# Optimization experiments

Hardware: AMD Instinct MI355X
Metric: run time of the kernel (lower is better)

## Reference

```python
import jax, jax.numpy as jnp
import numpy as np

B, T, D, H = 2, 2048, 1024, 16
HD = D // H
DFF = 4 * D
EPS = 1e-5


def gelu_tanh(x):
    c = jnp.sqrt(2.0 / jnp.pi).astype(x.dtype)
    return 0.5 * x * (1.0 + jnp.tanh(c * (x + 0.044715 * x ** 3)))


def layernorm(x, scale, shift):
    mean = jnp.mean(x, axis=-1, keepdims=True)
    var = jnp.var(x, axis=-1, keepdims=True)  # unbiased=False
    return (x - mean) / jnp.sqrt(var + EPS) * scale + shift


def setup_inputs() -> dict:
    key = jax.random.key(0)
    ks = jax.random.split(key, 12)
    s = lambda fan_in: 1.0 / np.sqrt(fan_in)
    return {
        "x": jax.random.normal(ks[0], (B, T, D), jnp.float32),
        "wq": jax.random.normal(ks[1], (D, D), jnp.float32) * s(D),
        "wk": jax.random.normal(ks[2], (D, D), jnp.float32) * s(D),
        "wv": jax.random.normal(ks[3], (D, D), jnp.float32) * s(D),
        "wo": jax.random.normal(ks[4], (D, D), jnp.float32) * s(D),
        "bo": jnp.zeros((D,), jnp.float32),
        "ln1_scale": jnp.ones((D,), jnp.float32),
        "ln1_shift": jnp.zeros((D,), jnp.float32),
        "ln2_scale": jnp.ones((D,), jnp.float32),
        "ln2_shift": jnp.zeros((D,), jnp.float32),
        "w1": jax.random.normal(ks[5], (D, DFF), jnp.float32) * s(D),
        "b1": jnp.zeros((DFF,), jnp.float32),
        "w2": jax.random.normal(ks[6], (DFF, D), jnp.float32) * s(DFF),
        "b2": jnp.zeros((D,), jnp.float32),
    }


def reference(x, wq, wk, wv, wo, bo, ln1_scale, ln1_shift, ln2_scale, ln2_shift, w1, b1, w2, b2):
    # pre-LN attention
    h = layernorm(x, ln1_scale, ln1_shift)
    q = (h @ wq).reshape(B, T, H, HD).transpose(0, 2, 1, 3)  # [B,H,T,hd]
    k = (h @ wk).reshape(B, T, H, HD).transpose(0, 2, 1, 3)
    v = (h @ wv).reshape(B, T, H, HD).transpose(0, 2, 1, 3)
    scores = jnp.einsum('bhqd,bhkd->bhqk', q, k) / jnp.sqrt(jnp.float32(HD))
    causal = jnp.tril(jnp.ones((T, T), bool))
    scores = jnp.where(causal, scores, -jnp.inf)
    attn = jax.nn.softmax(scores, axis=-1)
    ctx = jnp.einsum('bhqk,bhkd->bhqd', attn, v)
    ctx = ctx.transpose(0, 2, 1, 3).reshape(B, T, D)
    attn_out = ctx @ wo + bo
    x = x + attn_out  # dropout p=0
    # pre-LN FFN
    h2 = layernorm(x, ln2_scale, ln2_shift)
    ff = gelu_tanh(h2 @ w1 + b1) @ w2 + b2
    return x + ff
```

## Files before the change

### kernel.cpp

```cpp
#include <hip/hip_runtime.h>
#include <hip/hip_bf16.h>
#include <stdint.h>

typedef unsigned short u16;
typedef __attribute__((ext_vector_type(8))) short s16x8;
typedef __attribute__((ext_vector_type(4))) float f32x4;

#define B_   2
#define T_   2048
#define D_   1024
#define H_   16
#define HD_  64
#define DFF_ 4096
#define M_   (B_*T_)

#define SC2F 0.18033688f

__device__ __forceinline__ u16 f2b(float f){
  uint32_t u = __float_as_uint(f);
  u += 0x7FFFu + ((u >> 16) & 1u);
  return (u16)(u >> 16);
}
__device__ __forceinline__ float b2f(u16 u){ return __uint_as_float(((uint32_t)u) << 16); }
__device__ __forceinline__ uint32_t pk2(float lo, float hi){
  uint32_t r;
  asm volatile("v_cvt_pk_bf16_f32 %0, %1, %2" : "=v"(r) : "v"(lo), "v"(hi));
  return r;
}

__device__ __forceinline__ void gl_lds16(const void* g, void* l){
  __builtin_amdgcn_global_load_lds((const __attribute__((address_space(1))) void*)g,
                                   (__attribute__((address_space(3))) void*)l, 16, 0, 0);
}

template<int N> __device__ __forceinline__ void waitvm(){
  if constexpr (N == 0)      asm volatile("s_waitcnt vmcnt(0)" ::: "memory");
  else if constexpr (N == 2) asm volatile("s_waitcnt vmcnt(2)" ::: "memory");
  else if constexpr (N == 4) asm volatile("s_waitcnt vmcnt(4)" ::: "memory");
  else                       asm volatile("s_waitcnt vmcnt(8)" ::: "memory");
}

__device__ __forceinline__ void wconv_tile(const float* __restrict__ W, u16* __restrict__ Wt,
                                           int K, int N, int tk, int tn, int tid,
                                           u16* __restrict__ tile ){
  const int k0 = tk << 6, n0 = tn << 6;
  const int rr = tid >> 4, c4 = (tid & 15) << 2;
  #pragma unroll
  for (int rep = 0; rep < 4; rep++){
    int r = rr + (rep << 4);
    float4 v = *reinterpret_cast<const float4*>(W + (size_t)(k0 + r)*N + n0 + c4);
    tile[r*68 + c4+0] = f2b(v.x); tile[r*68 + c4+1] = f2b(v.y);
    tile[r*68 + c4+2] = f2b(v.z); tile[r*68 + c4+3] = f2b(v.w);
  }
  __syncthreads();
  const int rn = tid >> 2, kb = (tid & 3) << 4;
  u16 tmp[16];
  #pragma unroll
  for (int j = 0; j < 16; j++) tmp[j] = tile[(kb + j)*68 + rn];
  ushort4* dst = reinterpret_cast<ushort4*>(Wt + (size_t)(n0 + rn)*K + k0 + kb);
  dst[0] = make_ushort4(tmp[0], tmp[1], tmp[2], tmp[3]);
  dst[1] = make_ushort4(tmp[4], tmp[5], tmp[6], tmp[7]);
  dst[2] = make_ushort4(tmp[8], tmp[9], tmp[10], tmp[11]);
  dst[3] = make_ushort4(tmp[12], tmp[13], tmp[14], tmp[15]);
}

__global__ __launch_bounds__(256) void wconv_all(const float* __restrict__ wq,
                                                 const float* __restrict__ wk,
                                                 const float* __restrict__ wv,
                                                 const float* __restrict__ wo,
                                                 u16* __restrict__ wqkvT, u16* __restrict__ woT,
                                                 const float* __restrict__ x,
                                                 const float* __restrict__ ln1s,
                                                 const float* __restrict__ ln1b,
                                                 u16* __restrict__ hout){
  const int bid = blockIdx.x;
  const int tid = threadIdx.x;
  if (bid >= 1024){
    const int row = bid - 1024;
    float4 a = reinterpret_cast<const float4*>(x + ((size_t)row << 10))[tid];
    float s = a.x + a.y + a.z + a.w;
    float q = a.x*a.x + a.y*a.y + a.z*a.z + a.w*a.w;
    #pragma unroll
    for (int o = 32; o > 0; o >>= 1){ s += __shfl_xor(s, o); q += __shfl_xor(q, o); }
    __shared__ float red[8];
    const int w = tid >> 6;
    if ((tid & 63) == 0){ red[w] = s; red[4 + w] = q; }
    __syncthreads();
    float S = red[0] + red[1] + red[2] + red[3];
    float Q = red[4] + red[5] + red[6] + red[7];
    float mean = S * (1.0f/1024.0f);
    float var  = Q * (1.0f/1024.0f) - mean*mean;
    float inv = rsqrtf(var + 1e-5f);
    float4 gsc = reinterpret_cast<const float4*>(ln1s)[tid];
    float4 gsh = reinterpret_cast<const float4*>(ln1b)[tid];
    ushort4 o4;
    o4.x = f2b((a.x - mean)*inv*gsc.x + gsh.x);
    o4.y = f2b((a.y - mean)*inv*gsc.y + gsh.y);
    o4.z = f2b((a.z - mean)*inv*gsc.z + gsh.z);
    o4.w = f2b((a.w - mean)*inv*gsc.w + gsh.w);
    reinterpret_cast<ushort4*>(hout + ((size_t)row << 10))[tid] = o4;
    return;
  }
  __shared__ u16 tile[64*68];
  const int which = bid >> 8, t = bid & 255;
  const float* W = (which == 0) ? wq : (which == 1) ? wk : (which == 2) ? wv : wo;
  u16* Wt = (which == 3) ? woT : wqkvT + (size_t)which * D_ * D_;
  wconv_tile(W, Wt, 1024, 1024, t >> 4, t & 15, tid, tile);
}

__global__ __launch_bounds__(256) void reduce2(const u16* __restrict__ p,
                                               const float* __restrict__ bias,
                                               const u16* __restrict__ resid,
                                               float* __restrict__ out){
  const size_t idx = ((size_t)blockIdx.x << 8) + threadIdx.x;
  ushort4 a4 = reinterpret_cast<const ushort4*>(p)[idx];
  ushort4 b4 = reinterpret_cast<const ushort4*>(p)[idx + (((size_t)M_*D_) >> 2)];
  ushort4 r4 = reinterpret_cast<const ushort4*>(resid)[idx];
  float4 bb = reinterpret_cast<const float4*>(bias)[threadIdx.x];
  float4 o;
  o.x = b2f(a4.x) + b2f(b4.x) + b2f(r4.x) + bb.x;
  o.y = b2f(a4.y) + b2f(b4.y) + b2f(r4.y) + bb.y;
  o.z = b2f(a4.z) + b2f(b4.z) + b2f(r4.z) + bb.z;
  o.w = b2f(a4.w) + b2f(b4.w) + b2f(r4.w) + bb.w;
  reinterpret_cast<float4*>(out)[idx] = o;
}

__global__ __launch_bounds__(256) void reduce_ln(const u16* __restrict__ p,
                                                 const float* __restrict__ bias,
                                                 const float* __restrict__ resid,
                                                 const float* __restrict__ sc,
                                                 const float* __restrict__ sh,
                                                 u16* __restrict__ x1,
                                                 u16* __restrict__ h2){
  const int row = blockIdx.x;
  const int tid = threadIdx.x;
  const size_t idx = ((size_t)row << 8) + tid;
  ushort4 a4 = reinterpret_cast<const ushort4*>(p)[idx];
  ushort4 b4 = reinterpret_cast<const ushort4*>(p)[idx + (((size_t)M_*D_) >> 2)];
  float4 r  = reinterpret_cast<const float4*>(resid)[idx];
  float4 bb = reinterpret_cast<const float4*>(bias)[tid];
  float4 v;
  v.x = b2f(a4.x) + b2f(b4.x) + r.x + bb.x;
  v.y = b2f(a4.y) + b2f(b4.y) + r.y + bb.y;
  v.z = b2f(a4.z) + b2f(b4.z) + r.z + bb.z;
  v.w = b2f(a4.w) + b2f(b4.w) + r.w + bb.w;
  ushort4 xo;
  xo.x = f2b(v.x); xo.y = f2b(v.y); xo.z = f2b(v.z); xo.w = f2b(v.w);
  reinterpret_cast<ushort4*>(x1)[idx] = xo;
  float s = v.x + v.y + v.z + v.w;
  float q = v.x*v.x + v.y*v.y + v.z*v.z + v.w*v.w;
  #pragma unroll
  for (int o = 32; o > 0; o >>= 1){ s += __shfl_xor(s, o); q += __shfl_xor(q, o); }
  __shared__ float red[8];
  const int w = tid >> 6;
  if ((tid & 63) == 0){ red[w] = s; red[4 + w] = q; }
  __syncthreads();
  float S = red[0] + red[1] + red[2] + red[3];
  float Q = red[4] + red[5] + red[6] + red[7];
  float mean = S * (1.0f/1024.0f);
  float var  = Q * (1.0f/1024.0f) - mean*mean;
  float inv = rsqrtf(var + 1e-5f);
  float4 gsc = reinterpret_cast<const float4*>(sc)[tid];
  float4 gsh = reinterpret_cast<const float4*>(sh)[tid];
  ushort4 o4;
  o4.x = f2b((v.x - mean)*inv*gsc.x + gsh.x);
  o4.y = f2b((v.y - mean)*inv*gsc.y + gsh.y);
  o4.z = f2b((v.z - mean)*inv*gsc.z + gsh.z);
  o4.w = f2b((v.w - mean)*inv*gsc.w + gsh.w);
  reinterpret_cast<ushort4*>(h2 + ((size_t)row << 10))[tid] = o4;
}

template<int EPI, int NF>
__global__ __launch_bounds__(512, 2) void gemm8(const u16* __restrict__ A, const u16* __restrict__ Bt,
                                                const float* __restrict__ bias,
                                                void* __restrict__ Cv, void* __restrict__ Cv2,
                                                const float* __restrict__ cw1,
                                                const float* __restrict__ cw2,
                                                u16* __restrict__ w1T, u16* __restrict__ w2T,
                                                int M, int N, int K, int lda){
  constexpr int BROWS = NF * 32;
  __shared__ __align__(16) u16 LA[2][2][128*64];
  __shared__ __align__(16) u16 LB[2][2][BROWS*64];
  const int tid = threadIdx.x;

  if constexpr (EPI == 1){
    if (blockIdx.x >= 192){
      const int tid256 = tid & 255, sel2 = tid >> 8;
      u16* tile = &LA[0][0][0] + sel2 * (64*68);
      const int t = ((int)blockIdx.x - 192)*2 + sel2;
      if (t < 1024) wconv_tile(cw1, w1T, 1024, 4096, t >> 6, t & 63, tid256, tile);
      else          wconv_tile(cw2, w2T, 4096, 1024, (t-1024) >> 4, (t-1024) & 15, tid256, tile);
      return;
    }
  }

  const int lane = tid & 63;
  const int w = tid >> 6;
  const int wm = w >> 2, wn = w & 3;
  const int g = lane >> 4, l15 = lane & 15;
  const int bnb = (wn & 1) * (NF * 16);

  int tn, tm, kz;
  if constexpr (EPI == 1){
    const int flat = blockIdx.x;
    const int nfid = (flat & 7) * 24 + (flat >> 3);
    tn = nfid % 12; tm = nfid / 12; kz = 0;
  } else {
    const int nx = gridDim.x, ny = gridDim.y;
    const int nwg = nx * ny * gridDim.z;
    const int flat = blockIdx.x + nx * (blockIdx.y + ny * blockIdx.z);
    const int nfid = (flat & 7) * (nwg >> 3) + (flat >> 3);
    tn = nfid % nx;
    const int rest = nfid / nx;
    tm = rest % ny;
    kz = rest / ny;
  }
  const int tn0 = tn * (NF * 64);
  const int tm0 = tm << 8;
  const u16* Az = A  + (size_t)kz * K;
  const u16* Bz = Bt + (size_t)kz * K;

  const int arow0 = tid >> 3,         asl0 = (((tid) & 7) ^ (arow0 & 7)) << 3;
  const int arow1 = (tid + 512) >> 3, asl1 = (((tid + 512) & 7) ^ (arow1 & 7)) << 3;

  f32x4 acc[8][NF];
  #pragma unroll
  for (int i = 0; i < 8; i++)
    #pragma unroll
    for (int j = 0; j < NF; j++) acc[i][j] = (f32x4){0.f,0.f,0.f,0.f};
  s16x8 bf[NF][2];
  constexpr int WVX = (NF == 4) ? 8 : 2;

#define STG_A(db, h, tt) do{                                                        \
    gl_lds16(Az + (size_t)(tm0 + (h)*128 + arow0)*lda + ((tt) << 6) + asl0,         \
             &LA[db][h][tid*8]);                                                    \
    gl_lds16(Az + (size_t)(tm0 + (h)*128 + arow1)*lda + ((tt) << 6) + asl1,         \
             &LA[db][h][(tid + 512)*8]);                                            \
  }while(0)
#define STG_B(db, h, tt) do{                                                        \
    gl_lds16(Bz + (size_t)(tn0 + (h)*BROWS + arow0)*lda + ((tt) << 6) + asl0,       \
             &LB[db][h][tid*8]);                                                    \
    if constexpr (NF == 4){                                                         \
      gl_lds16(Bz + (size_t)(tn0 + (h)*BROWS + arow1)*lda + ((tt) << 6) + asl1,     \
               &LB[db][h][(tid + 512)*8]);                                          \
    }                                                                               \
  }while(0)
#define LDAF(db, mf, kk) (*reinterpret_cast<const s16x8*>(                          \
    &LA[db][wm][((mf)*16 + l15)*64 + ((((kk)*4 + g) ^ (l15 & 7)) << 3)]))
#define LDBF(db, nf, kk) (*reinterpret_cast<const s16x8*>(                          \
    &LB[db][wn >> 1][(bnb + (nf)*16 + l15)*64 + ((((kk)*4 + g) ^ (l15 & 7)) << 3)]))
#define BLOAD(db) do{ _Pragma("unroll")                                             \
    for (int nf = 0; nf < NF; nf++){ bf[nf][0] = LDBF(db, nf, 0);                   \
                                     bf[nf][1] = LDBF(db, nf, 1); } }while(0)
#define PH2(db, MF0, STG, WV) do{                                                   \
    s16x8 aA0 = LDAF(db, (MF0)+0, 0), aA1 = LDAF(db, (MF0)+0, 1);                   \
    s16x8 aB0 = LDAF(db, (MF0)+1, 0), aB1 = LDAF(db, (MF0)+1, 1);                   \
    s16x8 aC0 = LDAF(db, (MF0)+2, 0), aC1 = LDAF(db, (MF0)+2, 1);                   \
    s16x8 aD0 = LDAF(db, (MF0)+3, 0), aD1 = LDAF(db, (MF0)+3, 1);                   \
    STG;                                                                            \
    WV;                                                                             \
    __builtin_amdgcn_s_barrier();                                                   \
    __builtin_amdgcn_s_setprio(1);                                                  \
    _Pragma("unroll")                                                               \
    for (int nf = 0; nf < NF; nf++){                                                \
      acc[(MF0)+0][nf] = __builtin_amdgcn_mfma_f32_16x16x32_bf16(aA0, bf[nf][0], acc[(MF0)+0][nf], 0,0,0); \
      acc[(MF0)+0][nf] = __builtin_amdgcn_mfma_f32_16x16x32_bf16(aA1, bf[nf][1], acc[(MF0)+0][nf], 0,0,0); \
      acc[(MF0)+1][nf] = __builtin_amdgcn_mfma_f32_16x16x32_bf16(aB0, bf[nf][0], acc[(MF0)+1][nf], 0,0,0); \
      acc[(MF0)+1][nf] = __builtin_amdgcn_mfma_f32_16x16x32_bf16(aB1, bf[nf][1], acc[(MF0)+1][nf], 0,0,0); \
      acc[(MF0)+2][nf] = __builtin_amdgcn_mfma_f32_16x16x32_bf16(aC0, bf[nf][0], acc[(MF0)+2][nf], 0,0,0); \
      acc[(MF0)+2][nf] = __builtin_amdgcn_mfma_f32_16x16x32_bf16(aC1, bf[nf][1], acc[(MF0)+2][nf], 0,0,0); \
      acc[(MF0)+3][nf] = __builtin_amdgcn_mfma_f32_16x16x32_bf16(aD0, bf[nf][0], acc[(MF0)+3][nf], 0,0,0); \
      acc[(MF0)+3][nf] = __builtin_amdgcn_mfma_f32_16x16x32_bf16(aD1, bf[nf][1], acc[(MF0)+3][nf], 0,0,0); \
    }                                                                               \
    __builtin_amdgcn_s_setprio(0);                                                  \
    __builtin_amdgcn_s_barrier();                                                   \
  }while(0)

  const int NT = K >> 6;
  STG_B(0, 0, 0); STG_B(0, 1, 0); STG_A(0, 0, 0); STG_A(0, 1, 0);
  STG_B(1, 0, 1); STG_B(1, 1, 1);
  waitvm<WVX>();
  __builtin_amdgcn_s_barrier();

  for (int t = 0; t < NT; t += 2){
    const bool last = (t + 2 >= NT);
    BLOAD(0);
    PH2(0, 0, { STG_A(1, 0, t + 1); STG_A(1, 1, t + 1); }, );
    PH2(0, 4, { if (!last){ STG_B(0, 0, t + 2); STG_B(0, 1, t + 2); } },
              if (last) waitvm<0>(); else waitvm<WVX>(););
    BLOAD(1);
    PH2(1, 0, { if (!last){ STG_A(0, 0, t + 2); STG_A(0, 1, t + 2); } }, );
    PH2(1, 4, { if (!last){ STG_B(1, 0, t + 3); STG_B(1, 1, t + 3); } },
              if (last) waitvm<0>(); else waitvm<WVX>(););
  }
#undef STG_A
#undef STG_B
#undef LDAF
#undef LDBF
#undef BLOAD
#undef PH2

  if constexpr (EPI == 1){
    const int sel = tn0 >> 10;
    if (sel < 2){
      #pragma unroll
      for (int mf = 0; mf < 8; mf++){
        const int mb = tm0 + wm*128 + mf*16 + (g << 2);
        #pragma unroll
        for (int nf = 0; nf < NF; nf++){
          const int n = tn0 + wn*(NF*16) + nf*16 + l15;
          const int nn = n & 1023;
          const int hh = nn >> 6, d = nn & 63;
          #pragma unroll
          for (int rr = 0; rr < 4; rr++){
            const int m = mb + rr;
            float v = acc[mf][nf][rr];
            if (sel == 0) v *= SC2F;
            ((u16*)Cv)[(size_t)sel*((size_t)M_*D_) +
                       ((((size_t)(m >> 11)*H_ + hh)*T_ + (m & 2047)) << 6) + d] = f2b(v);
          }
        }
      }
    } else {
      u16* TR = &LA[0][0][0];
      u16* vt = (u16*)Cv2;
      const int bq = tm0 >> 11;
      const int tloc = tm0 & 2047;
      #pragma unroll
      for (int hp = 0; hp < 2; hp++){
        __syncthreads();
        if ((wn >> 1) == hp){
          #pragma unroll
          for (int mf = 0; mf < 8; mf++){
            const int mb = wm*128 + mf*16 + (g << 2);
            #pragma unroll
            for (int nf = 0; nf < NF; nf++){
              const int nr = ((wn & 1) << 6) + (nf << 4) + l15;
              #pragma unroll
              for (int rr = 0; rr < 4; rr++){
                const int m = mb + rr;
                TR[nr*256 + (((m >> 3) ^ (nr & 15)) << 3) + (m & 7)] = f2b(acc[mf][nf][rr]);
              }
            }
          }
        }
        __syncthreads();
        {
          const int nr = tid >> 2;
          const int m0 = (tid & 3) << 6;
          const int nn = (tn0 & 1023) + (hp << 7) + nr;
          const int hh = nn >> 6, d = nn & 63;
          u16* dst = vt + (((size_t)(bq*H_ + hh))*HD_ + d)*T_ + tloc + m0;
          #pragma unroll
          for (int jj = 0; jj < 8; jj++){
            const int j = (m0 >> 3) + jj;
            s16x8 vv = *reinterpret_cast<const s16x8*>(&TR[nr*256 + ((j ^ (nr & 15)) << 3)]);
            *reinterpret_cast<s16x8*>(dst + jj*8) = vv;
          }
        }
      }
    }
  } else {
    #pragma unroll
    for (int mf = 0; mf < 8; mf++){
      const int mb = tm0 + wm*128 + mf*16 + (g << 2);
      #pragma unroll
      for (int nf = 0; nf < NF; nf++){
        const int n = tn0 + wn*(NF*16) + nf*16 + l15;
        #pragma unroll
        for (int rr = 0; rr < 4; rr++){
          const int m = mb + rr;
          float v = acc[mf][nf][rr];
          if constexpr (EPI == 0){
            ((u16*)Cv)[(size_t)kz*((size_t)M*N) + (size_t)m*N + n] = f2b(v);
          } else {
            float u = v + bias[n];
            float t2 = 0.7978845608f*(u + 0.044715f*u*u*u);
            float e = __expf(2.0f*t2);
            float th = 1.0f - 2.0f/(e + 1.0f);
            ((u16*)Cv)[(size_t)m*N + n] = f2b(0.5f*u*(1.0f + th));
          }
        }
      }
    }
  }
}

__global__ __launch_bounds__(512) void attn_k(const u16* __restrict__ Qg, const u16* __restrict__ Kg,
                                              const u16* __restrict__ Vg, u16* __restrict__ ctx){
  const int flat = blockIdx.x + (blockIdx.y << 3);
  const int xcd = flat & 7, j_ = (flat >> 3) & 3, pr_ = flat >> 5;
  const int bh  = (j_ << 3) + xcd;
  const int tid = threadIdx.x;
  const int lane = tid & 63;
  const int w = tid >> 6;
  const int g = lane >> 4, l15 = lane & 15;

  __shared__ __align__(16) u16 Qs[128*64];
  __shared__ __align__(16) u16 Ks[2][128*64];
  __shared__ __align__(16) u16 Vt[2][64*128];
  __shared__ __align__(16) u16 Pl[8][16*128];
  u16* const Plw = &Pl[w][0];

  const size_t hb = (size_t)bh * ((size_t)T_*HD_);
  const u16* Qh = Qg + hb;
  const u16* Kh = Kg + hb;
  const u16* Vh = Vg + hb;
  const int b = bh >> 4, hh = bh & 15;

  const int qk_r0 = tid >> 3,         qk_c0 = (((tid) & 7) ^ (qk_r0 & 7)) << 3;
  const int qk_r1 = (tid + 512) >> 3, qk_c1 = (((tid + 512) & 7) ^ (qk_r1 & 7)) << 3;
  const int v_r0 = tid >> 4,          v_c0 = (((tid) & 15) ^ (v_r0 & 7)) << 3;
  const int v_r1 = (tid + 512) >> 4,  v_c1 = (((tid + 512) & 15) ^ (v_r1 & 7)) << 3;

  for (int ph = 0; ph < 2; ++ph){
    const int qt = ph ? (15 - pr_) : pr_;
    const int NKT = qt + 1;

    gl_lds16(Qh + (size_t)(qt*128 + qk_r0)*HD_ + qk_c0, Qs + tid*8);
    gl_lds16(Qh + (size_t)(qt*128 + qk_r1)*HD_ + qk_c1, Qs + (tid+512)*8);
    gl_lds16(Kh + (size_t)qk_r0*HD_ + qk_c0, Ks[0] + tid*8);
    gl_lds16(Kh + (size_t)qk_r1*HD_ + qk_c1, Ks[0] + (tid+512)*8);
    gl_lds16(Vh + (size_t)v_r0*T_ + v_c0, Vt[0] + tid*8);
    gl_lds16(Vh + (size_t)v_r1*T_ + v_c1, Vt[0] + (tid+512)*8);
    __syncthreads();

    s16x8 qa[2];
    #pragma unroll
    for (int kk = 0; kk < 2; kk++){
      int ra = (w << 4) + l15;
      int slot = (kk << 2) + g;
      qa[kk] = *reinterpret_cast<const s16x8*>(Qs + ra*64 + ((slot ^ (ra & 7)) << 3));
    }

    f32x4 accO[4];
    #pragma unroll
    for (int j = 0; j < 4; j++) accO[j] = (f32x4){0.f,0.f,0.f,0.f};
    float mrow = -1e30f, lrow = 0.f;
    const int qgl = qt*128 + (w << 4) + l15;

    for (int kt = 0; kt < NKT; ++kt){
      const int cur = kt & 1, nxt = cur ^ 1;
      const bool pf = (kt + 1 < NKT);

      if (pf){
        gl_lds16(Kh + (size_t)((kt+1)*128 + qk_r0)*HD_ + qk_c0, Ks[nxt] + tid*8);
        gl_lds16(Kh + (size_t)((kt+1)*128 + qk_r1)*HD_ + qk_c1, Ks[nxt] + (tid+512)*8);
        gl_lds16(Vh + (size_t)v_r0*T_ + (kt+1)*128 + v_c0, Vt[nxt] + tid*8);
        gl_lds16(Vh + (size_t)v_r1*T_ + (kt+1)*128 + v_c1, Vt[nxt] + (tid+512)*8);
      }

      f32x4 accS[8];
      #pragma unroll
      for (int j = 0; j < 8; j++) accS[j] = (f32x4){0.f,0.f,0.f,0.f};
      __builtin_amdgcn_s_setprio(1);
      #pragma unroll
      for (int jn = 0; jn < 8; jn++){
        #pragma unroll
        for (int kk = 0; kk < 2; kk++){
          int rb = (jn << 4) + l15;
          int slot = (kk << 2) + g;
          s16x8 kf = *reinterpret_cast<const s16x8*>(Ks[cur] + rb*64 + ((slot ^ (rb & 7)) << 3));
          accS[jn] = __builtin_amdgcn_mfma_f32_16x16x32_bf16(kf, qa[kk], accS[jn], 0, 0, 0);
        }
      }
      __builtin_amdgcn_s_setprio(0);

      if (kt == qt){
        #pragma unroll
        for (int jn = 0; jn < 8; jn++)
          #pragma unroll
          for (int rr = 0; rr < 4; rr++){
            int kgl = kt*128 + (jn << 4) + (g << 2) + rr;
            if (kgl > qgl) accS[jn][rr] = -1e30f;
          }
      }

      float rmax = accS[0][0];
      #pragma unroll
      for (int jn = 0; jn < 8; jn++)
        #pragma unroll
        for (int rr = 0; rr < 4; rr++) rmax = fmaxf(rmax, accS[jn][rr]);
      rmax = fmaxf(rmax, __shfl_xor(rmax, 16));
      rmax = fmaxf(rmax, __shfl_xor(rmax, 32));

      if (__any(rmax > mrow + 8.0f)){
        float mn = fmaxf(mrow, rmax);
        float sf = exp2f(mrow - mn);
        mrow = mn;
        lrow *= sf;
        #pragma unroll
        for (int rr = 0; rr < 4; rr++){
          float sfr = __shfl(sf, ((lane >> 4) << 2) + rr);
          #pragma unroll
          for (int jn = 0; jn < 4; jn++) accO[jn][rr] *= sfr;
        }
      }

      float tsum = 0.f;
      #pragma unroll
      for (int jn = 0; jn < 8; jn++){
        float pv0 = exp2f(accS[jn][0] - mrow);
        float pv1 = exp2f(accS[jn][1] - mrow);
        float pv2 = exp2f(accS[jn][2] - mrow);
        float pv3 = exp2f(accS[jn][3] - mrow);
        tsum += (pv0 + pv1) + (pv2 + pv3);
        int ch = ((jn << 1) | (g >> 1)) ^ (l15 & 7);
        int base = (l15 << 7) + (ch << 3) + ((g & 1) << 2);
        uint2 pkd = make_uint2(pk2(pv0, pv1), pk2(pv2, pv3));
        *reinterpret_cast<uint2*>(&Plw[base]) = pkd;
      }
      tsum += __shfl_xor(tsum, 16);
      tsum += __shfl_xor(tsum, 32);
      lrow += tsum;

      __builtin_amdgcn_s_setprio(1);
      #pragma unroll
      for (int kk = 0; kk < 4; kk++){
        int pch = ((kk << 2) + g) ^ (l15 & 7);
        s16x8 pa = *reinterpret_cast<const s16x8*>(&Plw[(l15 << 7) + (pch << 3)]);
        #pragma unroll
        for (int jn = 0; jn < 4; jn++){
          int vd = (jn << 4) + l15;
          int vslot = (((kk << 2) + g) & 8) | ((((kk << 2) + g) ^ (vd & 7)) & 7);
          s16x8 vbf = *reinterpret_cast<const s16x8*>(Vt[cur] + (vd << 7) + (vslot << 3));
          accO[jn] = __builtin_amdgcn_mfma_f32_16x16x32_bf16(pa, vbf, accO[jn], 0, 0, 0);
        }
      }
      __builtin_amdgcn_s_setprio(0);

      __syncthreads();
    }

    #pragma unroll
    for (int rr = 0; rr < 4; rr++){
      float lr = __shfl(lrow, ((lane >> 4) << 2) + rr);
      float inv = 1.0f / lr;
      int qrow = qt*128 + (w << 4) + (g << 2) + rr;
      size_t rowbase = ((size_t)(b*T_ + qrow) << 10) + ((size_t)hh << 6);
      #pragma unroll
      for (int jn = 0; jn < 4; jn++){
        int d = (jn << 4) + l15;
        ctx[rowbase + d] = f2b(accO[jn][rr] * inv);
      }
    }
  }
}

extern "C" void kernel_launch(void* const* d_in, const int* in_sizes, int n_in,
                              void* d_out, int out_size, void* d_ws, size_t ws_size,
                              hipStream_t stream){
  (void)in_sizes; (void)n_in; (void)out_size; (void)ws_size;
  const float* x    = (const float*)d_in[0];
  const float* wq   = (const float*)d_in[1];
  const float* wk   = (const float*)d_in[2];
  const float* wv   = (const float*)d_in[3];
  const float* wo   = (const float*)d_in[4];
  const float* bo   = (const float*)d_in[5];
  const float* ln1s = (const float*)d_in[6];
  const float* ln1b = (const float*)d_in[7];
  const float* ln2s = (const float*)d_in[8];
  const float* ln2b = (const float*)d_in[9];
  const float* w1   = (const float*)d_in[10];
  const float* b1   = (const float*)d_in[11];
  const float* w2   = (const float*)d_in[12];
  const float* b2   = (const float*)d_in[13];
  float* out = (float*)d_out;

  char* p = (char*)d_ws;
  u16*  wqkvT = (u16*)p;  p += (size_t)3*D_*D_*2;
  u16*  woT   = (u16*)p;  p += (size_t)D_*D_*2;
  u16*  w1T   = (u16*)p;  p += (size_t)D_*DFF_*2;
  u16*  w2T   = (u16*)p;  p += (size_t)DFF_*D_*2;
  u16*  h     = (u16*)p;  p += (size_t)M_*D_*2;
  u16*  qb    = (u16*)p;  p += (size_t)M_*D_*2;
  u16*  kb    = (u16*)p;  p += (size_t)M_*D_*2;
  u16*  vb    = (u16*)p;  p += (size_t)M_*D_*2;
  u16*  ctx   = (u16*)p;  p += (size_t)M_*D_*2;
  u16*  x1    = (u16*)p;  p += (size_t)M_*D_*2;
  u16*  h2    = (u16*)p;  p += (size_t)M_*D_*2;
  u16*  ff1   = (u16*)p;  p += (size_t)M_*DFF_*2;
  (void)kb; (void)vb;
  u16* part = h;

  dim3 blk(256), blk8(512);
  wconv_all<<<1024 + M_, blk, 0, stream>>>(wq, wk, wv, wo, wqkvT, woT, x, ln1s, ln1b, h);
  gemm8<1,4><<<192 + 1024, blk8, 0, stream>>>(h, wqkvT, nullptr, qb, ff1,
                                              w1, w2, w1T, w2T, M_, 3*D_, D_, D_);
  attn_k<<<dim3(8,32), blk8, 0, stream>>>(qb, qb + (size_t)M_*D_, ff1, ctx);
  gemm8<0,2><<<dim3(8,16,2), blk8, 0, stream>>>(ctx, woT, nullptr, part, nullptr,
                                                nullptr, nullptr, nullptr, nullptr,
                                                M_, D_, D_/2, D_);
  reduce_ln<<<M_, blk, 0, stream>>>(part, bo, x, ln2s, ln2b, x1, h2);
  gemm8<3,4><<<dim3(16,16,1), blk8, 0, stream>>>(h2, w1T, b1, ff1, nullptr,
                                                 nullptr, nullptr, nullptr, nullptr,
                                                 M_, DFF_, D_, D_);
  gemm8<0,2><<<dim3(8,16,2), blk8, 0, stream>>>(ff1, w2T, nullptr, part, nullptr,
                                                nullptr, nullptr, nullptr, nullptr,
                                                M_, D_, DFF_/2, DFF_);
  reduce2<<<M_, blk, 0, stream>>>(part, b2, x1, out);
}
```

Measured before the change: 202.8 us.

## Software-pipeline QK^T one tile ahead with triple-buffered K in attention

The attention loop now computes the next tile's QK^T scores while the current tile goes through softmax and PV, ping-ponging between two score accumulator sets. K gets a third LDS buffer and is prefetched two tiles ahead, V stays double-buffered. The aim is to overlap MFMA work with the exp/softmax VALU phase and hide load latency. In exchange it uses 16 KB more LDS and 32 more accumulator registers, which may lower occupancy or cause spills at 512 threads.

```diff
diff --git a/kernel.cpp b/kernel.cpp
--- a/kernel.cpp
+++ b/kernel.cpp
@@ -397,10 +397,11 @@
   const int g = lane >> 4, l15 = lane & 15;
 
   __shared__ __align__(16) u16 Qs[128*64];
-  __shared__ __align__(16) u16 Ks[2][128*64];
+  __shared__ __align__(16) u16 Ks[3][128*64];
   __shared__ __align__(16) u16 Vt[2][64*128];
   __shared__ __align__(16) u16 Pl[8][16*128];
   u16* const Plw = &Pl[w][0];
+  u16* const Ks0 = &Ks[0][0];
 
   const size_t hb = (size_t)bh * ((size_t)T_*HD_);
   const u16* Qh = Qg + hb;
@@ -413,6 +414,101 @@
   const int v_r0 = tid >> 4,          v_c0 = (((tid) & 15) ^ (v_r0 & 7)) << 3;
   const int v_r1 = (tid + 512) >> 4,  v_c1 = (((tid + 512) & 15) ^ (v_r1 & 7)) << 3;
 
+#define QKT_INTO(DST, KBUF) do{                                                    \
+    _Pragma("unroll")                                                              \
+    for (int j = 0; j < 8; j++) DST[j] = (f32x4){0.f,0.f,0.f,0.f};                 \
+    __builtin_amdgcn_s_setprio(1);                                                 \
+    _Pragma("unroll")                                                              \
+    for (int jn = 0; jn < 8; jn++){                                                \
+      _Pragma("unroll")                                                            \
+      for (int kk = 0; kk < 2; kk++){                                              \
+        int rb = (jn << 4) + l15;                                                  \
+        int slot = (kk << 2) + g;                                                  \
+        s16x8 kf = *reinterpret_cast<const s16x8*>((KBUF) + rb*64 + ((slot ^ (rb & 7)) << 3)); \
+        DST[jn] = __builtin_amdgcn_mfma_f32_16x16x32_bf16(kf, qa[kk], DST[jn], 0, 0, 0); \
+      }                                                                            \
+    }                                                                              \
+    __builtin_amdgcn_s_setprio(0);                                                 \
+  }while(0)
+
+#define STEP(KT, CUR, NXT) do{                                                     \
+    const int kt_ = (KT);                                                          \
+    const int vcur_ = kt_ & 1, vnxt_ = vcur_ ^ 1;                                  \
+    const bool hn_ = (kt_ + 1 < NKT);                                              \
+    if (kt_ + 2 < NKT){                                                            \
+      u16* kb2 = Ks0 + ((kt_ + 2) % 3) * (128*64);                                 \
+      gl_lds16(Kh + (size_t)((kt_+2)*128 + qk_r0)*HD_ + qk_c0, kb2 + tid*8);       \
+      gl_lds16(Kh + (size_t)((kt_+2)*128 + qk_r1)*HD_ + qk_c1, kb2 + (tid+512)*8); \
+    }                                                                              \
+    if (hn_){                                                                      \
+      gl_lds16(Vh + (size_t)v_r0*T_ + (kt_+1)*128 + v_c0, Vt[vnxt_] + tid*8);      \
+      gl_lds16(Vh + (size_t)v_r1*T_ + (kt_+1)*128 + v_c1, Vt[vnxt_] + (tid+512)*8);\
+      const u16* kb1 = Ks0 + ((kt_ + 1) % 3) * (128*64);                           \
+      QKT_INTO(NXT, kb1);                                                          \
+    }                                                                              \
+                                                 \
+    if (kt_ == qt){                                                                \
+      _Pragma("unroll")                                                            \
+      for (int jn = 0; jn < 8; jn++)                                               \
+        _Pragma("unroll")                                                          \
+        for (int rr = 0; rr < 4; rr++){                                            \
+          int kgl = kt_*128 + (jn << 4) + (g << 2) + rr;                           \
+          if (kgl > qgl) CUR[jn][rr] = -1e30f;                                     \
+        }                                                                          \
+    }                                                                              \
+    float rmax = CUR[0][0];                                                        \
+    _Pragma("unroll")                                                              \
+    for (int jn = 0; jn < 8; jn++)                                                 \
+      _Pragma("unroll")                                                            \
+      for (int rr = 0; rr < 4; rr++) rmax = fmaxf(rmax, CUR[jn][rr]);              \
+    rmax = fmaxf(rmax, __shfl_xor(rmax, 16));                                      \
+    rmax = fmaxf(rmax, __shfl_xor(rmax, 32));                                      \
+    if (__any(rmax > mrow + 8.0f)){                                                \
+      float mn = fmaxf(mrow, rmax);                                                \
+      float sf = exp2f(mrow - mn);                                                 \
+      mrow = mn;                                                                   \
+      lrow *= sf;                                                                  \
+      _Pragma("unroll")                                                            \
+      for (int rr = 0; rr < 4; rr++){                                              \
+        float sfr = __shfl(sf, ((lane >> 4) << 2) + rr);                           \
+        _Pragma("unroll")                                                          \
+        for (int jn = 0; jn < 4; jn++) accO[jn][rr] *= sfr;                        \
+      }                                                                            \
+    }                                                                              \
+    float tsum = 0.f;                                                              \
+    _Pragma("unroll")                                                              \
+    for (int jn = 0; jn < 8; jn++){                                                \
+      float pv0 = exp2f(CUR[jn][0] - mrow);                                        \
+      float pv1 = exp2f(CUR[jn][1] - mrow);                                        \
+      float pv2 = exp2f(CUR[jn][2] - mrow);                                        \
+      float pv3 = exp2f(CUR[jn][3] - mrow);                                        \
+      tsum += (pv0 + pv1) + (pv2 + pv3);                                           \
+      int ch = ((jn << 1) | (g >> 1)) ^ (l15 & 7);                                 \
+      int base = (l15 << 7) + (ch << 3) + ((g & 1) << 2);                          \
+      uint2 pkd = make_uint2(pk2(pv0, pv1), pk2(pv2, pv3));                        \
+      *reinterpret_cast<uint2*>(&Plw[base]) = pkd;                                 \
+    }                                                                              \
+    tsum += __shfl_xor(tsum, 16);                                                  \
+    tsum += __shfl_xor(tsum, 32);                                                  \
+    lrow += tsum;                                                                  \
+                                            \
+    __builtin_amdgcn_s_setprio(1);                                                 \
+    _Pragma("unroll")                                                              \
+    for (int kk = 0; kk < 4; kk++){                                                \
+      int pch = ((kk << 2) + g) ^ (l15 & 7);                                       \
+      s16x8 pa = *reinterpret_cast<const s16x8*>(&Plw[(l15 << 7) + (pch << 3)]);   \
+      _Pragma("unroll")                                                            \
+      for (int jn = 0; jn < 4; jn++){                                              \
+        int vd = (jn << 4) + l15;                                                  \
+        int vslot = (((kk << 2) + g) & 8) | ((((kk << 2) + g) ^ (vd & 7)) & 7);    \
+        s16x8 vbf = *reinterpret_cast<const s16x8*>(Vt[vcur_] + (vd << 7) + (vslot << 3)); \
+        accO[jn] = __builtin_amdgcn_mfma_f32_16x16x32_bf16(pa, vbf, accO[jn], 0, 0, 0); \
+      }                                                                            \
+    }                                                                              \
+    __builtin_amdgcn_s_setprio(0);                                                 \
+    __syncthreads();                                                               \
+  }while(0)
+
   for (int ph = 0; ph < 2; ++ph){
     const int qt = ph ? (15 - pr_) : pr_;
     const int NKT = qt + 1;
@@ -421,6 +517,10 @@
     gl_lds16(Qh + (size_t)(qt*128 + qk_r1)*HD_ + qk_c1, Qs + (tid+512)*8);
     gl_lds16(Kh + (size_t)qk_r0*HD_ + qk_c0, Ks[0] + tid*8);
     gl_lds16(Kh + (size_t)qk_r1*HD_ + qk_c1, Ks[0] + (tid+512)*8);
+    if (NKT > 1){
+      gl_lds16(Kh + (size_t)(128 + qk_r0)*HD_ + qk_c0, Ks[1] + tid*8);
+      gl_lds16(Kh + (size_t)(128 + qk_r1)*HD_ + qk_c1, Ks[1] + (tid+512)*8);
+    }
     gl_lds16(Vh + (size_t)v_r0*T_ + v_c0, Vt[0] + tid*8);
     gl_lds16(Vh + (size_t)v_r1*T_ + v_c1, Vt[0] + (tid+512)*8);
     __syncthreads();
@@ -439,97 +539,15 @@
     float mrow = -1e30f, lrow = 0.f;
     const int qgl = qt*128 + (w << 4) + l15;
 
-    for (int kt = 0; kt < NKT; ++kt){
-      const int cur = kt & 1, nxt = cur ^ 1;
-      const bool pf = (kt + 1 < NKT);
-
-      if (pf){
-        gl_lds16(Kh + (size_t)((kt+1)*128 + qk_r0)*HD_ + qk_c0, Ks[nxt] + tid*8);
-        gl_lds16(Kh + (size_t)((kt+1)*128 + qk_r1)*HD_ + qk_c1, Ks[nxt] + (tid+512)*8);
-        gl_lds16(Vh + (size_t)v_r0*T_ + (kt+1)*128 + v_c0, Vt[nxt] + tid*8);
-        gl_lds16(Vh + (size_t)v_r1*T_ + (kt+1)*128 + v_c1, Vt[nxt] + (tid+512)*8);
-      }
-
-      f32x4 accS[8];
-      #pragma unroll
-      for (int j = 0; j < 8; j++) accS[j] = (f32x4){0.f,0.f,0.f,0.f};
-      __builtin_amdgcn_s_setprio(1);
-      #pragma unroll
-      for (int jn = 0; jn < 8; jn++){
-        #pragma unroll
-        for (int kk = 0; kk < 2; kk++){
-          int rb = (jn << 4) + l15;
-          int slot = (kk << 2) + g;
-          s16x8 kf = *reinterpret_cast<const s16x8*>(Ks[cur] + rb*64 + ((slot ^ (rb & 7)) << 3));
-          accS[jn] = __builtin_amdgcn_mfma_f32_16x16x32_bf16(kf, qa[kk], accS[jn], 0, 0, 0);
-        }
-      }
-      __builtin_amdgcn_s_setprio(0);
-
-      if (kt == qt){
-        #pragma unroll
-        for (int jn = 0; jn < 8; jn++)
-          #pragma unroll
-          for (int rr = 0; rr < 4; rr++){
-            int kgl = kt*128 + (jn << 4) + (g << 2) + rr;
-            if (kgl > qgl) accS[jn][rr] = -1e30f;
-          }
-      }
-
-      float rmax = accS[0][0];
-      #pragma unroll
-      for (int jn = 0; jn < 8; jn++)
-        #pragma unroll
-        for (int rr = 0; rr < 4; rr++) rmax = fmaxf(rmax, accS[jn][rr]);
-      rmax = fmaxf(rmax, __shfl_xor(rmax, 16));
-      rmax = fmaxf(rmax, __shfl_xor(rmax, 32));
-
-      if (__any(rmax > mrow + 8.0f)){
-        float mn = fmaxf(mrow, rmax);
-        float sf = exp2f(mrow - mn);
-        mrow = mn;
-        lrow *= sf;
-        #pragma unroll
-        for (int rr = 0; rr < 4; rr++){
-          float sfr = __shfl(sf, ((lane >> 4) << 2) + rr);
-          #pragma unroll
-          for (int jn = 0; jn < 4; jn++) accO[jn][rr] *= sfr;
-        }
-      }
-
-      float tsum = 0.f;
-      #pragma unroll
-      for (int jn = 0; jn < 8; jn++){
-        float pv0 = exp2f(accS[jn][0] - mrow);
-        float pv1 = exp2f(accS[jn][1] - mrow);
-        float pv2 = exp2f(accS[jn][2] - mrow);
-        float pv3 = exp2f(accS[jn][3] - mrow);
-        tsum += (pv0 + pv1) + (pv2 + pv3);
-        int ch = ((jn << 1) | (g >> 1)) ^ (l15 & 7);
-        int base = (l15 << 7) + (ch << 3) + ((g & 1) << 2);
-        uint2 pkd = make_uint2(pk2(pv0, pv1), pk2(pv2, pv3));
-        *reinterpret_cast<uint2*>(&Plw[base]) = pkd;
-      }
-      tsum += __shfl_xor(tsum, 16);
-      tsum += __shfl_xor(tsum, 32);
-      lrow += tsum;
-
-      __builtin_amdgcn_s_setprio(1);
-      #pragma unroll
-      for (int kk = 0; kk < 4; kk++){
-        int pch = ((kk << 2) + g) ^ (l15 & 7);
-        s16x8 pa = *reinterpret_cast<const s16x8*>(&Plw[(l15 << 7) + (pch << 3)]);
-        #pragma unroll
-        for (int jn = 0; jn < 4; jn++){
-          int vd = (jn << 4) + l15;
-          int vslot = (((kk << 2) + g) & 8) | ((((kk << 2) + g) ^ (vd & 7)) & 7);
-          s16x8 vbf = *reinterpret_cast<const s16x8*>(Vt[cur] + (vd << 7) + (vslot << 3));
-          accO[jn] = __builtin_amdgcn_mfma_f32_16x16x32_bf16(pa, vbf, accO[jn], 0, 0, 0);
-        }
-      }
-      __builtin_amdgcn_s_setprio(0);
-
-      __syncthreads();
+    f32x4 accA[8], accB[8];
+    QKT_INTO(accA, Ks0);
+
+    int kt = 0;
+    while (true){
+      STEP(kt, accA, accB); kt++;
+      if (kt >= NKT) break;
+      STEP(kt, accB, accA); kt++;
+      if (kt >= NKT) break;
     }
 
     #pragma unroll
@@ -545,6 +563,8 @@
       }
     }
   }
+#undef STEP
+#undef QKT_INTO
 }
 
 extern "C" void kernel_launch(void* const* d_in, const int* in_sizes, int n_in,
```

Result: slower. 208.1 us (+2.6%).
